# Kernel tuning notes

Measured on AMD Instinct MI355X. Metric: run time of the kernel, lower is better.

The kernel has to match this reference:

```python
import jax, jax.numpy as jnp
import numpy as np

NUM_EXPERTS = 8
TOP_K = 2
B, S, H, I = 4, 2048, 2048, 1408
INIT = 0.02


def setup_inputs() -> dict:
    key = jax.random.key(0)
    ks = jax.random.split(key, 6)
    return {
        "selected_experts": jax.random.randint(ks[0], (B, S, TOP_K), 0, NUM_EXPERTS, dtype=jnp.int32),
        "hidden_states": jax.random.normal(ks[1], (B, S, H), dtype=jnp.float32),
        "routing_weights": jax.random.uniform(ks[2], (B, S, TOP_K), dtype=jnp.float32),
        "gate_w": jax.random.normal(ks[3], (NUM_EXPERTS, H, I), dtype=jnp.float32) * INIT,
        "up_w": jax.random.normal(ks[4], (NUM_EXPERTS, H, I), dtype=jnp.float32) * INIT,
        "down_w": jax.random.normal(ks[5], (NUM_EXPERTS, I, H), dtype=jnp.float32) * INIT,
        "batch_size": B,
        "sequence_length": S,
        "hidden_dim": H,
    }


def reference(selected_experts, hidden_states, routing_weights, gate_w, up_w, down_w,
              batch_size, sequence_length, hidden_dim):
    # Naive MoE: every expert's SwiGLU MLP runs on every token, then the
    # output is scaled by sum((selected_experts == e) * routing_weights, -1).
    num_experts = gate_w.shape[0]
    final = jnp.zeros_like(hidden_states)
    for e in range(num_experts):  # fixed small expert count, structurally a loop in the original
        g = jnp.einsum("bsh,hi->bsi", hidden_states, gate_w[e])
        u = jnp.einsum("bsh,hi->bsi", hidden_states, up_w[e])
        out = jnp.einsum("bsi,ih->bsh", jax.nn.silu(g) * u, down_w[e])
        w = jnp.sum(jnp.where(selected_experts == e, routing_weights, 0.0), axis=-1)  # [B,S]
        final = final + w[:, :, None] * out
    return final
```

## Files before the change

### kernel.cpp

```cpp
#include <hip/hip_runtime.h>
#include <stdint.h>

#define TT 8192
#define HH 2048
#define II 1408
#define NE 8
#define NROWS (TT*2)
#define BM 128
#define BK 64
#define BND 128
#define MAX_SLOTS 144
#define NKT_GU (HH/BK)
#define NKT_DN (II/BK)
#define NYT_GU (II/64)
#define NYT_DN (HH/BND)
#define SPX (MAX_SLOTS/8)

#define NB_CVT 8192
#define NB_T2  (22*32*16)
#define NB_TD  (32*22*8)
#define NB_Z   2048
#define B0_CVT 1
#define B0_T2  (B0_CVT + NB_CVT)
#define B0_TD  (B0_T2 + NB_T2)
#define B0_Z   (B0_TD + NB_TD)
#define NB_ALL (B0_Z + NB_Z)

typedef unsigned short u16;
typedef __attribute__((ext_vector_type(8))) __bf16 bhalf8;
typedef __attribute__((ext_vector_type(4))) float f32x4;
typedef __attribute__((ext_vector_type(4))) float float4v;
typedef __attribute__((ext_vector_type(4))) int int4v;

__device__ __forceinline__ u16 f2bf(float f) {
  union { float f; unsigned u; } v; v.f = f;
  return (u16)((v.u + 0x7FFFu + ((v.u >> 16) & 1u)) >> 16);
}

__device__ __forceinline__ void gld16(const void* g, void* l) {
  __builtin_amdgcn_global_load_lds(
      (const __attribute__((address_space(1))) unsigned int*)g,
      (__attribute__((address_space(3))) unsigned int*)l, 16, 0, 0);
}

__global__ __launch_bounds__(256) void k_prep(const int* __restrict__ sel,
                                              const float* __restrict__ rw,
                                              const float* __restrict__ hs,
                                              const float* __restrict__ gw,
                                              const float* __restrict__ uw,
                                              const float* __restrict__ dw,
                                              u16* __restrict__ hsb,
                                              u16* __restrict__ gwt,
                                              u16* __restrict__ uwt,
                                              u16* __restrict__ dwt,
                                              float* __restrict__ outz,
                                              int* __restrict__ token_idx,
                                              float* __restrict__ wrow,
                                              int* __restrict__ s_e,
                                              int* __restrict__ s_rs,
                                              int* __restrict__ s_rows) {
  int b = blockIdx.x;
  int tid = threadIdx.x;

  if (b == 0) {
    __shared__ int cnt[NE], offs[NE + 1], cursor[NE];
    if (tid < NE) cnt[tid] = 0;
    __syncthreads();
    for (int i = tid; i < NROWS; i += 256) atomicAdd(&cnt[sel[i]], 1);
    __syncthreads();
    if (tid == 0) {
      int o = 0;
      for (int e = 0; e < NE; ++e) { offs[e] = o; o += cnt[e]; }
      offs[NE] = o;
      int ns = 0;
      for (int e = 0; e < NE; ++e) {
        for (int t = 0; t < cnt[e]; t += BM) {
          s_e[ns] = e;
          s_rs[ns] = offs[e] + t;
          s_rows[ns] = (cnt[e] - t < BM) ? (cnt[e] - t) : BM;
          ns++;
        }
      }
      for (; ns < MAX_SLOTS; ++ns) s_rows[ns] = 0;
    }
    __syncthreads();
    if (tid < NE) cursor[tid] = offs[tid];
    __syncthreads();
    for (int i = tid; i < NROWS; i += 256) {
      int e = sel[i];
      int r = atomicAdd(&cursor[e], 1);
      token_idx[r] = i >> 1;
      wrow[r] = rw[i];
    }
    return;
  }

  if (b < B0_T2) {
    size_t i = ((size_t)(b - B0_CVT) * 256 + tid) * 8;
    float4v a = *(const float4v*)(hs + i);
    float4v c = *(const float4v*)(hs + i + 4);
    u16 o[8];
    o[0] = f2bf(a.x); o[1] = f2bf(a.y); o[2] = f2bf(a.z); o[3] = f2bf(a.w);
    o[4] = f2bf(c.x); o[5] = f2bf(c.y); o[6] = f2bf(c.z); o[7] = f2bf(c.w);
    *(int4v*)(hsb + i) = *(const int4v*)o;
    return;
  }

  if (b >= B0_Z) {
    int4v z = (int4v)0;
    size_t n4 = (size_t)TT * HH / 4;
    for (size_t i = (size_t)(b - B0_Z) * 256 + tid; i < n4; i += (size_t)NB_Z * 256)
      ((int4v*)outz)[i] = z;
    return;
  }

  __shared__ float t[64][65];
  const float* ip;
  u16* op;
  int R, C, r0, c0;
  if (b < B0_TD) {
    int idx = b - B0_T2;
    int x = idx % 22, y = (idx / 22) % 32, z = idx / (22 * 32);
    int e = z & 7;
    R = HH; C = II;
    ip = ((z < 8) ? gw : uw) + (size_t)e * R * C;
    op = ((z < 8) ? gwt : uwt) + (size_t)e * R * C;
    r0 = y * 64; c0 = x * 64;
  } else {
    int idx = b - B0_TD;
    int x = idx % 32, y = (idx / 32) % 22, z = idx / (32 * 22);
    R = II; C = HH;
    ip = dw + (size_t)z * R * C;
    op = dwt + (size_t)z * R * C;
    r0 = y * 64; c0 = x * 64;
  }
  int rr = tid >> 4, c4 = (tid & 15) * 4;
#pragma unroll
  for (int j = 0; j < 4; ++j) {
    float4v v = *(const float4v*)&ip[(size_t)(r0 + rr + 16 * j) * C + c0 + c4];
    t[rr + 16 * j][c4 + 0] = v.x;
    t[rr + 16 * j][c4 + 1] = v.y;
    t[rr + 16 * j][c4 + 2] = v.z;
    t[rr + 16 * j][c4 + 3] = v.w;
  }
  __syncthreads();
  int cc = tid >> 2, rb = (tid & 3) * 16;
  u16 buf[16];
#pragma unroll
  for (int i = 0; i < 16; ++i) buf[i] = f2bf(t[rb + i][cc]);
  u16* p = op + (size_t)(c0 + cc) * R + r0 + rb;
  *(int4v*)p = *(const int4v*)&buf[0];
  *(int4v*)(p + 8) = *(const int4v*)&buf[8];
}

__global__ __launch_bounds__(256, 4) void k_gu(const u16* __restrict__ hsb,
                                               const u16* __restrict__ gwt,
                                               const u16* __restrict__ uwt,
                                               const int* __restrict__ token_idx,
                                               const float* __restrict__ wrow,
                                               const int* __restrict__ s_e,
                                               const int* __restrict__ s_rs,
                                               const int* __restrict__ s_rows,
                                               u16* __restrict__ act) {
  int f = blockIdx.x;
  int xcd = f & 7;
  int pos = f >> 3;
  int slot = xcd * SPX + pos % SPX;
  int ytile = pos / SPX;
  int nrows = s_rows[slot];
  if (nrows == 0) return;
  int e = s_e[slot];
  int row0 = s_rs[slot];
  int i0 = ytile * 64;

  __shared__ alignas(16) u16 As[BM][BK];
  __shared__ alignas(16) u16 Bg[64][BK];
  __shared__ alignas(16) u16 Bu[64][BK];

  int tid = threadIdx.x;
  int lane = tid & 63;
  int wid = tid >> 6;
  int l8 = lane >> 3;
  int c8 = lane & 7;
  int cs = c8 ^ l8;

  const u16* agp[4];
#pragma unroll
  for (int j = 0; j < 4; ++j) {
    int gr = row0 + wid * 32 + j * 8 + l8;
    if (gr > NROWS - 1) gr = NROWS - 1;
    int tok = token_idx[gr];
    agp[j] = hsb + (size_t)tok * HH + cs * 8;
  }
  const u16* ggp[2]; const u16* ugp[2];
#pragma unroll
  for (int j = 0; j < 2; ++j) {
    size_t off = ((size_t)e * II + i0 + wid * 16 + j * 8 + l8) * HH + cs * 8;
    ggp[j] = gwt + off;
    ugp[j] = uwt + off;
  }

  int wm = wid >> 1, wn = wid & 1;
  int l15 = lane & 15, l16 = lane >> 4;

  f32x4 accg[4][2], accu[4][2];
#pragma unroll
  for (int a = 0; a < 4; ++a)
#pragma unroll
    for (int b = 0; b < 2; ++b) { accg[a][b] = (f32x4)0.0f; accu[a][b] = (f32x4)0.0f; }

  for (int kt = 0; kt < NKT_GU; ++kt) {
    int k0 = kt * BK;
#pragma unroll
    for (int j = 0; j < 4; ++j) gld16(agp[j] + k0, &As[wid * 32 + j * 8][0]);
#pragma unroll
    for (int j = 0; j < 2; ++j) {
      gld16(ggp[j] + k0, &Bg[wid * 16 + j * 8][0]);
      gld16(ugp[j] + k0, &Bu[wid * 16 + j * 8][0]);
    }
    __syncthreads();
#pragma unroll
    for (int ks = 0; ks < 2; ++ks) {
      bhalf8 af[4], bgf[2], buf_[2];
#pragma unroll
      for (int mf = 0; mf < 4; ++mf) {
        int row = wm * 64 + mf * 16 + l15;
        int c = (ks * 4 + l16) ^ (row & 7);
        af[mf] = *(const bhalf8*)&As[row][c * 8];
      }
#pragma unroll
      for (int nf = 0; nf < 2; ++nf) {
        int row = wn * 32 + nf * 16 + l15;
        int c = (ks * 4 + l16) ^ (row & 7);
        bgf[nf] = *(const bhalf8*)&Bg[row][c * 8];
        buf_[nf] = *(const bhalf8*)&Bu[row][c * 8];
      }
#pragma unroll
      for (int mf = 0; mf < 4; ++mf)
#pragma unroll
        for (int nf = 0; nf < 2; ++nf) {
          accg[mf][nf] = __builtin_amdgcn_mfma_f32_16x16x32_bf16(af[mf], bgf[nf], accg[mf][nf], 0, 0, 0);
          accu[mf][nf] = __builtin_amdgcn_mfma_f32_16x16x32_bf16(af[mf], buf_[nf], accu[mf][nf], 0, 0, 0);
        }
    }
    __syncthreads();
  }

#pragma unroll
  for (int mf = 0; mf < 4; ++mf) {
#pragma unroll
    for (int j = 0; j < 4; ++j) {
      int lm = wm * 64 + mf * 16 + l16 * 4 + j;
      if (lm < nrows) {
        int gr = row0 + lm;
        float w = wrow[gr];
        size_t base = (size_t)gr * II + i0 + wn * 32 + l15;
#pragma unroll
        for (int nf = 0; nf < 2; ++nf) {
          float g = accg[mf][nf][j];
          float u = accu[mf][nf][j];
          float s = g / (1.0f + __expf(-g));
          act[base + nf * 16] = f2bf(s * u * w);
        }
      }
    }
  }
}

__global__ __launch_bounds__(256, 3) void k_down(const u16* __restrict__ act,
                                                 const u16* __restrict__ dwt,
                                                 const int* __restrict__ token_idx,
                                                 const int* __restrict__ s_e,
                                                 const int* __restrict__ s_rs,
                                                 const int* __restrict__ s_rows,
                                                 float* __restrict__ out) {
  int f = blockIdx.x;
  int xcd = f & 7;
  int pos = f >> 3;
  int slot = xcd * SPX + pos % SPX;
  int ytile = pos / SPX;
  int nrows = s_rows[slot];
  if (nrows == 0) return;
  int e = s_e[slot];
  int row0 = s_rs[slot];
  int h0 = ytile * BND;

  __shared__ alignas(16) u16 As[BM][BK];
  __shared__ alignas(16) u16 Bs[BND][BK];

  int tid = threadIdx.x;
  int lane = tid & 63;
  int wid = tid >> 6;
  int l8 = lane >> 3;
  int c8 = lane & 7;
  int cs = c8 ^ l8;

  const u16* agp[4];
#pragma unroll
  for (int j = 0; j < 4; ++j) {
    int gr = row0 + wid * 32 + j * 8 + l8;
    if (gr > NROWS - 1) gr = NROWS - 1;
    agp[j] = act + (size_t)gr * II + cs * 8;
  }
  const u16* bgp[4];
#pragma unroll
  for (int j = 0; j < 4; ++j)
    bgp[j] = dwt + ((size_t)e * HH + h0 + wid * 32 + j * 8 + l8) * II + cs * 8;

  int wm = wid >> 1, wn = wid & 1;
  int l15 = lane & 15, l16 = lane >> 4;

  f32x4 acc[4][4];
#pragma unroll
  for (int a = 0; a < 4; ++a)
#pragma unroll
    for (int b = 0; b < 4; ++b) acc[a][b] = (f32x4)0.0f;

  for (int kt = 0; kt < NKT_DN; ++kt) {
    int k0 = kt * BK;
#pragma unroll
    for (int j = 0; j < 4; ++j) {
      gld16(agp[j] + k0, &As[wid * 32 + j * 8][0]);
      gld16(bgp[j] + k0, &Bs[wid * 32 + j * 8][0]);
    }
    __syncthreads();
#pragma unroll
    for (int ks = 0; ks < 2; ++ks) {
      bhalf8 af[4], bf[4];
#pragma unroll
      for (int mf = 0; mf < 4; ++mf) {
        int row = wm * 64 + mf * 16 + l15;
        int c = (ks * 4 + l16) ^ (row & 7);
        af[mf] = *(const bhalf8*)&As[row][c * 8];
      }
#pragma unroll
      for (int nf = 0; nf < 4; ++nf) {
        int row = wn * 64 + nf * 16 + l15;
        int c = (ks * 4 + l16) ^ (row & 7);
        bf[nf] = *(const bhalf8*)&Bs[row][c * 8];
      }
#pragma unroll
      for (int mf = 0; mf < 4; ++mf)
#pragma unroll
        for (int nf = 0; nf < 4; ++nf)
          acc[mf][nf] = __builtin_amdgcn_mfma_f32_16x16x32_bf16(af[mf], bf[nf], acc[mf][nf], 0, 0, 0);
    }
    __syncthreads();
  }

#pragma unroll
  for (int mf = 0; mf < 4; ++mf) {
#pragma unroll
    for (int j = 0; j < 4; ++j) {
      int lm = wm * 64 + mf * 16 + l16 * 4 + j;
      if (lm < nrows) {
        int tok = token_idx[row0 + lm];
        size_t base = (size_t)tok * HH + h0 + wn * 64 + l15;
#pragma unroll
        for (int nf = 0; nf < 4; ++nf)
          atomicAdd(&out[base + nf * 16], acc[mf][nf][j]);
      }
    }
  }
}

extern "C" void kernel_launch(void* const* d_in, const int* in_sizes, int n_in,
                              void* d_out, int out_size, void* d_ws, size_t ws_size,
                              hipStream_t stream) {
  const int* sel = (const int*)d_in[0];
  const float* hs = (const float*)d_in[1];
  const float* rw = (const float*)d_in[2];
  const float* gw = (const float*)d_in[3];
  const float* uw = (const float*)d_in[4];
  const float* dw = (const float*)d_in[5];
  float* out = (float*)d_out;

  char* ws = (char*)d_ws;
  size_t o = 0;
  u16* hsb = (u16*)(ws + o); o += (size_t)TT * HH * 2;
  u16* gwt = (u16*)(ws + o); o += (size_t)NE * HH * II * 2;
  u16* uwt = (u16*)(ws + o); o += (size_t)NE * HH * II * 2;
  u16* dwt = (u16*)(ws + o); o += (size_t)NE * HH * II * 2;
  u16* act = (u16*)(ws + o); o += (size_t)NROWS * II * 2;
  int* token_idx = (int*)(ws + o); o += (size_t)NROWS * 4;
  float* wrow = (float*)(ws + o); o += (size_t)NROWS * 4;
  int* s_e = (int*)(ws + o); o += MAX_SLOTS * 4;
  int* s_rs = (int*)(ws + o); o += MAX_SLOTS * 4;
  int* s_rows = (int*)(ws + o); o += MAX_SLOTS * 4;
  (void)ws_size; (void)in_sizes; (void)n_in; (void)out_size;

  k_prep<<<NB_ALL, 256, 0, stream>>>(sel, rw, hs, gw, uw, dw,
                                     hsb, gwt, uwt, dwt, out,
                                     token_idx, wrow, s_e, s_rs, s_rows);

  k_gu<<<MAX_SLOTS * NYT_GU, 256, 0, stream>>>(hsb, gwt, uwt, token_idx, wrow,
                                               s_e, s_rs, s_rows, act);

  k_down<<<MAX_SLOTS * NYT_DN, 256, 0, stream>>>(act, dwt, token_idx,
                                                 s_e, s_rs, s_rows, out);
}
```

Baseline: 538.7 us.

## Move down-weight transpose and output zeroing into gate/up kernel tail blocks

The down-projection weight transpose/bf16 conversion and the output zero-fill move out of the prep kernel into extra blocks appended to the gate/up GEMM launch. This shortens the prep kernel's critical path and lets that memory-bound work overlap with the gate/up GEMM, which only needs data k_down consumes later. The zero-fill block count also drops. The cost is a grid-stride zero loop per block and shared memory changed to a union-style buffer, which could affect GEMM occupancy or the block scheduling mix.

```diff
diff --git a/kernel.cpp b/kernel.cpp
--- a/kernel.cpp
+++ b/kernel.cpp
@@ -18,13 +18,14 @@
 
 #define NB_CVT 8192
 #define NB_T2  (22*32*16)
-#define NB_TD  (32*22*8)
-#define NB_Z   2048
 #define B0_CVT 1
 #define B0_T2  (B0_CVT + NB_CVT)
-#define B0_TD  (B0_T2 + NB_T2)
-#define B0_Z   (B0_TD + NB_TD)
-#define NB_ALL (B0_Z + NB_Z)
+#define NB_PREP (B0_T2 + NB_T2)
+
+#define NBG (MAX_SLOTS*NYT_GU)
+#define NB_TD (32*22*8)
+#define NB_Z  512
+#define NBG_ALL (NBG + NB_TD + NB_Z)
 
 typedef unsigned short u16;
 typedef __attribute__((ext_vector_type(8))) __bf16 bhalf8;
@@ -48,12 +49,9 @@
                                               const float* __restrict__ hs,
                                               const float* __restrict__ gw,
                                               const float* __restrict__ uw,
-                                              const float* __restrict__ dw,
                                               u16* __restrict__ hsb,
                                               u16* __restrict__ gwt,
                                               u16* __restrict__ uwt,
-                                              u16* __restrict__ dwt,
-                                              float* __restrict__ outz,
                                               int* __restrict__ token_idx,
                                               float* __restrict__ wrow,
                                               int* __restrict__ s_e,
@@ -106,34 +104,14 @@
     return;
   }
 
-  if (b >= B0_Z) {
-    int4v z = (int4v)0;
-    size_t n4 = (size_t)TT * HH / 4;
-    for (size_t i = (size_t)(b - B0_Z) * 256 + tid; i < n4; i += (size_t)NB_Z * 256)
-      ((int4v*)outz)[i] = z;
-    return;
-  }
-
   __shared__ float t[64][65];
-  const float* ip;
-  u16* op;
-  int R, C, r0, c0;
-  if (b < B0_TD) {
-    int idx = b - B0_T2;
-    int x = idx % 22, y = (idx / 22) % 32, z = idx / (22 * 32);
-    int e = z & 7;
-    R = HH; C = II;
-    ip = ((z < 8) ? gw : uw) + (size_t)e * R * C;
-    op = ((z < 8) ? gwt : uwt) + (size_t)e * R * C;
-    r0 = y * 64; c0 = x * 64;
-  } else {
-    int idx = b - B0_TD;
-    int x = idx % 32, y = (idx / 32) % 22, z = idx / (32 * 22);
-    R = II; C = HH;
-    ip = dw + (size_t)z * R * C;
-    op = dwt + (size_t)z * R * C;
-    r0 = y * 64; c0 = x * 64;
-  }
+  int idx = b - B0_T2;
+  int x = idx % 22, y = (idx / 22) % 32, z = idx / (22 * 32);
+  int e = z & 7;
+  const int R = HH, C = II;
+  const float* ip = ((z < 8) ? gw : uw) + (size_t)e * R * C;
+  u16* op = ((z < 8) ? gwt : uwt) + (size_t)e * R * C;
+  int r0 = y * 64, c0 = x * 64;
   int rr = tid >> 4, c4 = (tid & 15) * 4;
 #pragma unroll
   for (int j = 0; j < 4; ++j) {
@@ -161,8 +139,54 @@
                                                const int* __restrict__ s_e,
                                                const int* __restrict__ s_rs,
                                                const int* __restrict__ s_rows,
-                                               u16* __restrict__ act) {
+                                               u16* __restrict__ act,
+                                               const float* __restrict__ dw,
+                                               u16* __restrict__ dwt,
+                                               float* __restrict__ outz) {
+  __shared__ alignas(16) char smem[32768];
   int f = blockIdx.x;
+  int tid = threadIdx.x;
+
+  if (f >= NBG) {
+    int b = f - NBG;
+    if (b < NB_TD) {
+      float (*t)[65] = (float(*)[65])smem;
+      int x = b % 32, y = (b / 32) % 22, z = b / (32 * 22);
+      const int R = II, C = HH;
+      const float* ip = dw + (size_t)z * R * C;
+      u16* op = dwt + (size_t)z * R * C;
+      int r0 = y * 64, c0 = x * 64;
+      int rr = tid >> 4, c4 = (tid & 15) * 4;
+#pragma unroll
+      for (int j = 0; j < 4; ++j) {
+        float4v v = *(const float4v*)&ip[(size_t)(r0 + rr + 16 * j) * C + c0 + c4];
+        t[rr + 16 * j][c4 + 0] = v.x;
+        t[rr + 16 * j][c4 + 1] = v.y;
+        t[rr + 16 * j][c4 + 2] = v.z;
+        t[rr + 16 * j][c4 + 3] = v.w;
+      }
+      __syncthreads();
+      int cc = tid >> 2, rb = (tid & 3) * 16;
+      u16 buf[16];
+#pragma unroll
+      for (int i = 0; i < 16; ++i) buf[i] = f2bf(t[rb + i][cc]);
+      u16* p = op + (size_t)(c0 + cc) * R + r0 + rb;
+      *(int4v*)p = *(const int4v*)&buf[0];
+      *(int4v*)(p + 8) = *(const int4v*)&buf[8];
+    } else {
+      int4v zv = (int4v)0;
+      size_t n4 = (size_t)TT * HH / 4;
+      for (size_t i = (size_t)(b - NB_TD) * 256 + tid; i < n4;
+           i += (size_t)NB_Z * 256)
+        ((int4v*)outz)[i] = zv;
+    }
+    return;
+  }
+
+  u16 (*As)[BK] = (u16(*)[BK])(smem);
+  u16 (*Bg)[BK] = (u16(*)[BK])(smem + 16384);
+  u16 (*Bu)[BK] = (u16(*)[BK])(smem + 24576);
+
   int xcd = f & 7;
   int pos = f >> 3;
   int slot = xcd * SPX + pos % SPX;
@@ -173,11 +197,6 @@
   int row0 = s_rs[slot];
   int i0 = ytile * 64;
 
-  __shared__ alignas(16) u16 As[BM][BK];
-  __shared__ alignas(16) u16 Bg[64][BK];
-  __shared__ alignas(16) u16 Bu[64][BK];
-
-  int tid = threadIdx.x;
   int lane = tid & 63;
   int wid = tid >> 6;
   int l8 = lane >> 3;
@@ -207,7 +226,7 @@
 #pragma unroll
   for (int a = 0; a < 4; ++a)
 #pragma unroll
-    for (int b = 0; b < 2; ++b) { accg[a][b] = (f32x4)0.0f; accu[a][b] = (f32x4)0.0f; }
+    for (int b2 = 0; b2 < 2; ++b2) { accg[a][b2] = (f32x4)0.0f; accu[a][b2] = (f32x4)0.0f; }
 
   for (int kt = 0; kt < NKT_GU; ++kt) {
     int k0 = kt * BK;
@@ -389,12 +408,12 @@
   int* s_rows = (int*)(ws + o); o += MAX_SLOTS * 4;
   (void)ws_size; (void)in_sizes; (void)n_in; (void)out_size;
 
-  k_prep<<<NB_ALL, 256, 0, stream>>>(sel, rw, hs, gw, uw, dw,
-                                     hsb, gwt, uwt, dwt, out,
-                                     token_idx, wrow, s_e, s_rs, s_rows);
-
-  k_gu<<<MAX_SLOTS * NYT_GU, 256, 0, stream>>>(hsb, gwt, uwt, token_idx, wrow,
-                                               s_e, s_rs, s_rows, act);
+  k_prep<<<NB_PREP, 256, 0, stream>>>(sel, rw, hs, gw, uw,
+                                      hsb, gwt, uwt,
+                                      token_idx, wrow, s_e, s_rs, s_rows);
+
+  k_gu<<<NBG_ALL, 256, 0, stream>>>(hsb, gwt, uwt, token_idx, wrow,
+                                    s_e, s_rs, s_rows, act, dw, dwt, out);
 
   k_down<<<MAX_SLOTS * NYT_DN, 256, 0, stream>>>(act, dwt, token_idx,
                                                  s_e, s_rs, s_rows, out);
```

New measurement: 530.9 us. About the same (-1.4%).
